# Kernel tuning notes

Measured on AMD Instinct MI355X. Metric: run time of the kernel, lower is better.

## Reference

```python
import jax, jax.numpy as jnp
import numpy as np
import math
from itertools import combinations

SEQ_LEN = 8
SET_SIZE = 3
IN_DIM = 2048
OUT_DIM = 1152
WAY = 5
SHOT = 5
N_QUERIES = 200
PE_SCALE = 0.1
LN_EPS = 1e-5
NEG_INF = -1e30

TUPLES = np.array(list(combinations(range(SEQ_LEN), SET_SIZE)), dtype=np.int32)  # [56, 3]
TUPLES_LEN = TUPLES.shape[0]


def _positional_encoding(d_model, max_len):
    position = np.arange(max_len)[:, None].astype(np.float32)
    div_term = np.exp(np.arange(0, d_model, 2).astype(np.float32) * -(math.log(10000.0) / d_model))
    pe = np.zeros((max_len, d_model), dtype=np.float32)
    pe[:, 0::2] = np.sin(position * div_term) * PE_SCALE
    pe[:, 1::2] = np.cos(position * div_term) * PE_SCALE
    return jnp.asarray(pe)

PE = _positional_encoding(IN_DIM, int(SEQ_LEN * 1.5))


def setup_inputs() -> dict:
    key = jax.random.key(0)
    ks = jax.random.split(key, 6)
    support_set = jax.random.normal(ks[0], (WAY * SHOT, SEQ_LEN, IN_DIM), dtype=jnp.float32)
    queries = jax.random.normal(ks[1], (N_QUERIES, SEQ_LEN, IN_DIM), dtype=jnp.float32)
    support_labels = jnp.repeat(jnp.arange(WAY, dtype=jnp.int32), SHOT)  # [25]
    Wk = jax.random.normal(ks[2], (IN_DIM * SET_SIZE, OUT_DIM), dtype=jnp.float32) * 0.02
    bk = jnp.zeros((OUT_DIM,), dtype=jnp.float32)
    Wv = jax.random.normal(ks[3], (IN_DIM * SET_SIZE, OUT_DIM), dtype=jnp.float32) * 0.02
    bv = jnp.zeros((OUT_DIM,), dtype=jnp.float32)
    ln_g = jnp.ones((OUT_DIM,), dtype=jnp.float32)
    ln_b = jnp.zeros((OUT_DIM,), dtype=jnp.float32)
    return {"support_set": support_set, "support_labels": support_labels, "queries": queries,
            "Wk": Wk, "bk": bk, "Wv": Wv, "bv": bv, "ln_g": ln_g, "ln_b": ln_b}


def _layernorm(x, g, b):
    mu = jnp.mean(x, axis=-1, keepdims=True)
    var = jnp.var(x, axis=-1, keepdims=True)
    return (x - mu) * jax.lax.rsqrt(var + LN_EPS) * g + b


def _tuple_features(x):
    # x: [N, SEQ_LEN, IN_DIM]; add PE (dropout is identity at inference), gather frame tuples.
    n = x.shape[0]
    x = x + PE[None, :x.shape[1], :]
    return x[:, TUPLES, :].reshape(n, TUPLES_LEN, SET_SIZE * IN_DIM)  # [N, 56, 6144]


def reference(support_set, support_labels, queries, Wk, bk, Wv, bv, ln_g, ln_b):
    n_q = queries.shape[0]
    s_feat = _tuple_features(support_set)   # [S, T, 6144]
    q_feat = _tuple_features(queries)       # [Q, T, 6144]

    sk = _layernorm(s_feat @ Wk + bk, ln_g, ln_b)  # [S, T, D]
    qk = _layernorm(q_feat @ Wk + bk, ln_g, ln_b)  # [Q, T, D]
    sv = s_feat @ Wv + bv                           # [S, T, D]
    qv = q_feat @ Wv + bv                           # [Q, T, D]

    # scores between every query tuple and every support tuple
    scores = jnp.einsum('qtd,skd->qtsk', qk, sk) / math.sqrt(OUT_DIM)  # [Q, T, S, T]

    # per-class masked softmax over (support clips of class c) x (support tuples)
    class_mask = support_labels[None, :] == jnp.arange(WAY, dtype=support_labels.dtype)[:, None]  # [WAY, S]
    masked = scores[None] + jnp.where(class_mask[:, None, None, :, None], 0.0, NEG_INF)  # [WAY, Q, T, S, T]
    attn = jax.nn.softmax(masked.reshape(WAY, n_q, TUPLES_LEN, -1), axis=-1)
    attn = attn.reshape(WAY, n_q, TUPLES_LEN, -1, TUPLES_LEN)  # [WAY, Q, T, S, T]

    proto = jnp.einsum('cqtsk,skd->cqtd', attn, sv)  # [WAY, Q, T, D]
    diff = qv[None] - proto                           # [WAY, Q, T, D]
    dist = -jnp.sum(diff * diff, axis=(2, 3)) / TUPLES_LEN  # [WAY, Q]
    return dist.T  # logits [Q, WAY]
```

## Files before the change

### kernel.cpp

```cpp
#include <hip/hip_runtime.h>
#include <math.h>

#define SEQ_LEN 8
#define IN_DIM 2048
#define OUT_DIM 1152
#define NTUP 56
#define NSUP 25
#define NQ 200
#define WAY 5
#define SFRAMES 200
#define NFRAMES 1800
#define SROWS 1400
#define QROWS 11200
#define AT_STRIDE 1440
#define KC 288
#define ALD 296

typedef __attribute__((ext_vector_type(8))) short short8;
typedef __attribute__((ext_vector_type(4))) float f32x4;

__device__ __constant__ int TUP[NTUP][3] = {
{0,1,2},{0,1,3},{0,1,4},{0,1,5},{0,1,6},{0,1,7},
{0,2,3},{0,2,4},{0,2,5},{0,2,6},{0,2,7},
{0,3,4},{0,3,5},{0,3,6},{0,3,7},
{0,4,5},{0,4,6},{0,4,7},
{0,5,6},{0,5,7},
{0,6,7},
{1,2,3},{1,2,4},{1,2,5},{1,2,6},{1,2,7},
{1,3,4},{1,3,5},{1,3,6},{1,3,7},
{1,4,5},{1,4,6},{1,4,7},
{1,5,6},{1,5,7},
{1,6,7},
{2,3,4},{2,3,5},{2,3,6},{2,3,7},
{2,4,5},{2,4,6},{2,4,7},
{2,5,6},{2,5,7},
{2,6,7},
{3,4,5},{3,4,6},{3,4,7},
{3,5,6},{3,5,7},
{3,6,7},
{4,5,6},{4,5,7},
{4,6,7},
{5,6,7}};

__device__ __forceinline__ unsigned short f2bf(float x) {
  union { float f; unsigned int u; } v; v.f = x;
  unsigned int r = v.u + 0x7fffu + ((v.u >> 16) & 1u);
  return (unsigned short)(r >> 16);
}
__device__ __forceinline__ float bf2f(unsigned short s) {
  union { float f; unsigned int u; } v; v.u = ((unsigned int)s) << 16;
  return v.f;
}

__device__ __forceinline__ void gll16(const void* g, void* l) {
  __builtin_amdgcn_global_load_lds(
      (const __attribute__((address_space(1))) unsigned int*)g,
      (__attribute__((address_space(3))) unsigned int*)l, 16, 0, 0);
}

#define VMCNT(N) asm volatile("s_waitcnt vmcnt(" #N ")" ::: "memory")

__device__ __forceinline__ void pbar() {
  asm volatile("" ::: "memory");
  __builtin_amdgcn_s_barrier();
  asm volatile("" ::: "memory");
}

#define APB_OFF   0UL
#define WT_OFF    7372800UL
#define PB_OFF    35684352UL
#define QKB_OFF   60567552UL
#define SKB_OFF   86372352UL
#define PVB_OFF   102039552UL
#define H_OFF     102061312UL
#define SVB_OFF   115402752UL
#define G2_OFF    118628352UL
#define SCB_OFF   119457792UL
#define G1B_OFF   151713792UL
#define QNORM_OFF 183969792UL
#define RANK_OFF  184014592UL

__global__ __launch_bounds__(256) void k_pre(const float* __restrict__ S,
                                             const float* __restrict__ Q,
                                             const float* __restrict__ Wk,
                                             const float* __restrict__ Wv,
                                             const int* __restrict__ labels,
                                             unsigned short* __restrict__ APb,
                                             unsigned short* __restrict__ WT,
                                             int* __restrict__ rank,
                                             float* __restrict__ outz) {
  __shared__ float t[32][33];
  int b = blockIdx.x, tid = threadIdx.x;
  if (b < NFRAMES) {
    int frame = b;
    int e8 = tid * 8;
    int pos = frame & 7;
    const float c0 = -logf(10000.0f) / (float)IN_DIM;
    float pe[8];
#pragma unroll
    for (int p = 0; p < 4; ++p) {
      float dt = expf((float)(e8 + 2 * p) * c0);
      float arg = (float)pos * dt;
      pe[2 * p] = sinf(arg) * 0.1f;
      pe[2 * p + 1] = cosf(arg) * 0.1f;
    }
    const float* src = (frame < SFRAMES) ? (S + (size_t)frame * IN_DIM + e8)
                                         : (Q + (size_t)(frame - SFRAMES) * IN_DIM + e8);
    float4 x0 = ((const float4*)src)[0], x1 = ((const float4*)src)[1];
    short8 o;
    o[0] = (short)f2bf(x0.x + pe[0]); o[1] = (short)f2bf(x0.y + pe[1]);
    o[2] = (short)f2bf(x0.z + pe[2]); o[3] = (short)f2bf(x0.w + pe[3]);
    o[4] = (short)f2bf(x1.x + pe[4]); o[5] = (short)f2bf(x1.y + pe[5]);
    o[6] = (short)f2bf(x1.z + pe[6]); o[7] = (short)f2bf(x1.w + pe[7]);
    *(short8*)(APb + (size_t)frame * IN_DIM + e8) = o;
  } else if (b < NFRAMES + 13824) {
    int z = b - NFRAMES;
    int bz = z / (64 * 36); int rem = z % (64 * 36);
    int by = rem / 64, bx = rem % 64;
    int w = bz / 3, j = bz % 3;
    const float* W = w ? Wv : Wk;
    int k0 = bx * 32, d0 = by * 32;
    int tx = tid & 31, ty = tid >> 5;
#pragma unroll
    for (int i = 0; i < 4; ++i) {
      int k = k0 + ty + i * 8;
      t[ty + i * 8][tx] = W[(size_t)(j * IN_DIM + k) * OUT_DIM + d0 + tx];
    }
    __syncthreads();
    int colbase = w * 3456 + j * 1152 + d0;
#pragma unroll
    for (int i = 0; i < 4; ++i) {
      int d = ty + i * 8;
      WT[(size_t)(colbase + d) * IN_DIM + k0 + tx] = f2bf(t[tx][d]);
    }
  } else {
    for (int i = tid; i < NQ * WAY; i += 256) outz[i] = 0.f;
    if (tid == 0) {
      for (int s = 0; s < NSUP; ++s) {
        int r = 0;
        for (int s2 = 0; s2 < NSUP; ++s2)
          r += (labels[s2] < labels[s]) || (labels[s2] == labels[s] && s2 < s);
        rank[s] = r;
      }
    }
  }
}

__device__ __forceinline__ void mfma_core256p(const short* a0p, const short* a1p,
                                              const short* a2p, const short* a3p,
                                              const short* b0p, const short* b1p,
                                              int K, short* lds, f32x4 (&acc)[8][4]) {
  int tid = threadIdx.x;
  int lane = tid & 63, wave = tid >> 6;
  int wm = wave >> 1, wn = wave & 1;
  int col = lane & 15, quad = lane >> 4;
  int kq8 = (quad ^ ((col >> 1) & 3)) * 8;
  const int nt = K >> 5;

#define STAGE(t, cb)                                 \
  do {                                               \
    short* buf_ = lds + (cb);                        \
    int k0_ = (t) << 5;                              \
    gll16(a0p + k0_, buf_ + (size_t)tid * 8);        \
    gll16(a1p + k0_, buf_ + (size_t)(tid + 256) * 8);\
    gll16(a2p + k0_, buf_ + (size_t)(tid + 512) * 8);\
    gll16(a3p + k0_, buf_ + (size_t)(tid + 768) * 8);\
    gll16(b0p + k0_, buf_ + 8192 + (size_t)tid * 8); \
    gll16(b1p + k0_, buf_ + 8192 + (size_t)(tid + 256) * 8);\
  } while (0)

  STAGE(0, 0);
  STAGE(1, 12288);
  VMCNT(6);
  pbar();
  int c0 = 0, c1 = 12288, c2 = 24576;
  for (int t = 0; t < nt; ++t) {
    if (t + 2 < nt) STAGE(t + 2, c2);
    const short* As = lds + c0;
    const short* Bs = As + 8192;
    short8 af[8], bf[4];
#pragma unroll
    for (int i = 0; i < 8; ++i)
      af[i] = *(const short8*)(As + (wm * 128 + i * 16 + col) * 32 + kq8);
#pragma unroll
    for (int j = 0; j < 4; ++j)
      bf[j] = *(const short8*)(Bs + (wn * 64 + j * 16 + col) * 32 + kq8);
    __builtin_amdgcn_s_setprio(1);
#pragma unroll
    for (int i = 0; i < 8; ++i)
#pragma unroll
      for (int j = 0; j < 4; ++j)
        acc[i][j] = __builtin_amdgcn_mfma_f32_16x16x32_bf16(af[i], bf[j], acc[i][j], 0, 0, 0);
    __builtin_amdgcn_s_setprio(0);
    if (t + 2 < nt)      VMCNT(6);
    else if (t + 1 < nt) VMCNT(0);
    pbar();
    int tmp = c0; c0 = c1; c1 = c2; c2 = tmp;
  }
#undef STAGE
}

__device__ __forceinline__ void mfma_core256(const short* __restrict__ A, int lda, int maxA,
                                             const short* __restrict__ B, int ldb, int maxB,
                                             int K, short* lds, f32x4 (&acc)[8][4]) {
  int tid = threadIdx.x;
  int rt_ = tid >> 2;
  int qo = ((tid & 3) ^ ((tid >> 3) & 3)) * 8;
  mfma_core256p(A + (size_t)min(rt_,       maxA) * lda + qo,
                A + (size_t)min(rt_ + 64,  maxA) * lda + qo,
                A + (size_t)min(rt_ + 128, maxA) * lda + qo,
                A + (size_t)min(rt_ + 192, maxA) * lda + qo,
                B + (size_t)min(rt_,       maxB) * ldb + qo,
                B + (size_t)min(rt_ + 64,  maxB) * ldb + qo,
                K, lds, acc);
}

__global__ __launch_bounds__(256, 2) void k_gemm1(const unsigned short* __restrict__ APb,
                                                  const unsigned short* __restrict__ WT,
                                                  unsigned short* __restrict__ Pb) {
  __shared__ short lds[36864];
  int o = blockIdx.x;
  int L = (o & 7) * 54 + (o >> 3);
  int rt = L / 54, ct = L % 54;
  int row0 = rt << 8, col0 = ct << 7;
  f32x4 acc[8][4];
#pragma unroll
  for (int i = 0; i < 8; ++i)
#pragma unroll
    for (int j = 0; j < 4; ++j) acc[i][j] = (f32x4)(0.f);
  mfma_core256((const short*)APb + (size_t)row0 * IN_DIM, IN_DIM, min(255, NFRAMES - 1 - row0),
               (const short*)WT + (size_t)col0 * IN_DIM, IN_DIM, 127,
               IN_DIM, lds, acc);
  int lane = threadIdx.x & 63, wave = threadIdx.x >> 6;
  int wm = wave >> 1, wn = wave & 1, col = lane & 15, quad = lane >> 4;
#pragma unroll
  for (int i = 0; i < 8; ++i)
#pragma unroll
    for (int r = 0; r < 4; ++r) {
      int gr = row0 + wm * 128 + i * 16 + quad * 4 + r;
      if (gr >= NFRAMES) continue;
#pragma unroll
      for (int j = 0; j < 4; ++j)
        Pb[(size_t)gr * 6912 + col0 + wn * 64 + j * 16 + col] = f2bf(acc[i][j][r]);
    }
}

__global__ __launch_bounds__(256) void k_pvb(const unsigned short* __restrict__ Pb,
                                             const float* __restrict__ bv,
                                             float* __restrict__ pvb) {
  int fr = blockIdx.x, tid = threadIdx.x;
  int wave = tid >> 6, lane = tid & 63;
  if (wave < 3) {
    const unsigned short* src = Pb + (size_t)fr * 6912 + 3456 + wave * 1152;
    float s = 0.f;
    for (int k = lane; k < OUT_DIM; k += 64) s += bf2f(src[k]) * bv[k];
#pragma unroll
    for (int o = 32; o; o >>= 1) s += __shfl_xor(s, o);
    if (lane == 0) pvb[fr * 3 + wave] = s;
  }
}

__global__ __launch_bounds__(256) void k_combine(const unsigned short* __restrict__ Pb,
                                                 const float* __restrict__ bk,
                                                 const float* __restrict__ bv,
                                                 const float* __restrict__ g,
                                                 const float* __restrict__ bb,
                                                 const int* __restrict__ rank,
                                                 unsigned short* __restrict__ SKb,
                                                 unsigned short* __restrict__ QKb,
                                                 unsigned short* __restrict__ SVb,
                                                 float* __restrict__ qnorm) {
  __shared__ short L[8 * 3456];
  int n = blockIdx.x, w = blockIdx.y;
  int tid = threadIdx.x;
  bool sup = n < NSUP;
  int fbase = sup ? n * SEQ_LEN : SFRAMES + (n - NSUP) * SEQ_LEN;
  for (int i = 0; i < 14; ++i) {
    int idx = tid + 256 * i;
    if (idx < 3456) {
      int fr = idx / 432, off = (idx - fr * 432) * 8;
      *(short8*)(L + fr * 3456 + off) =
          *(const short8*)(Pb + (size_t)(fbase + fr) * 6912 + w * 3456 + off);
    }
  }
  __syncthreads();
  int wave = tid >> 6, lane = tid & 63;
  const float* bias = w ? bv : bk;
  float2 bi[9], gg[9], bbv[9];
#pragma unroll
  for (int i = 0; i < 9; ++i) {
    int p = lane + 64 * i;
    bi[i] = *(const float2*)(bias + 2 * p);
    if (w == 0) {
      gg[i] = *(const float2*)(g + 2 * p);
      bbv[i] = *(const float2*)(bb + 2 * p);
    }
  }
  int obase = sup ? rank[n] * NTUP : (n - NSUP) * NTUP;
  const unsigned int* Lu = (const unsigned int*)L;
  for (int t = wave; t < NTUP; t += 4) {
    int b0 = (TUP[t][0] * 3456) >> 1;
    int b1 = (TUP[t][1] * 3456 + 1152) >> 1;
    int b2 = (TUP[t][2] * 3456 + 2304) >> 1;
    float va[18];
    float sum = 0.f, sq = 0.f;
#pragma unroll
    for (int i = 0; i < 9; ++i) {
      int p = lane + 64 * i;
      unsigned int u0 = Lu[b0 + p], u1 = Lu[b1 + p], u2 = Lu[b2 + p];
      float a = bf2f((unsigned short)u0) + bf2f((unsigned short)u1) +
                bf2f((unsigned short)u2) + bi[i].x;
      float b = bf2f((unsigned short)(u0 >> 16)) + bf2f((unsigned short)(u1 >> 16)) +
                bf2f((unsigned short)(u2 >> 16)) + bi[i].y;
      va[2 * i] = a; va[2 * i + 1] = b;
      sum += a + b;
      sq += a * a + b * b;
    }
#pragma unroll
    for (int o = 32; o; o >>= 1) {
      sum += __shfl_xor(sum, o);
      sq += __shfl_xor(sq, o);
    }
    int orow = obase + t;
    if (w == 0) {
      float mean = sum * (1.f / OUT_DIM);
      float var = sq * (1.f / OUT_DIM) - mean * mean;
      float inv = rsqrtf(var + 1e-5f);
      unsigned short* outp = (sup ? SKb : QKb) + (size_t)orow * OUT_DIM;
#pragma unroll
      for (int i = 0; i < 9; ++i) {
        int p = lane + 64 * i;
        unsigned int lo = f2bf((va[2 * i] - mean) * inv * gg[i].x + bbv[i].x);
        unsigned int hi = f2bf((va[2 * i + 1] - mean) * inv * gg[i].y + bbv[i].y);
        *(unsigned int*)(outp + 2 * p) = lo | (hi << 16);
      }
    } else if (sup) {
      unsigned short* outp = SVb + (size_t)orow * OUT_DIM;
#pragma unroll
      for (int i = 0; i < 9; ++i) {
        int p = lane + 64 * i;
        unsigned int lo = f2bf(va[2 * i]);
        unsigned int hi = f2bf(va[2 * i + 1]);
        *(unsigned int*)(outp + 2 * p) = lo | (hi << 16);
      }
    } else {
      if (lane == 0) qnorm[orow] = sq;
    }
  }
}

__global__ __launch_bounds__(256, 2) void k_rowgemm(const unsigned short* __restrict__ QKb,
                                                    const unsigned short* __restrict__ SKb,
                                                    const unsigned short* __restrict__ SVb,
                                                    const unsigned short* __restrict__ Pb,
                                                    unsigned short* __restrict__ SCb,
                                                    float* __restrict__ H,
                                                    unsigned short* __restrict__ G2) {
  __shared__ short lds[36864];
  int o = blockIdx.x;
  int xcd = o & 7, idx = o >> 3;
  int L = (xcd == 0 ? idx : 77 + (xcd - 1) * 76 + idx);
  f32x4 acc[8][4];
#pragma unroll
  for (int i = 0; i < 8; ++i)
#pragma unroll
    for (int j = 0; j < 4; ++j) acc[i][j] = (f32x4)(0.f);
  int lane = threadIdx.x & 63, wave = threadIdx.x >> 6;
  int wm = wave >> 1, wn = wave & 1, col = lane & 15, quad = lane >> 4;

  if (L < 484) {
    int rt = L / 11, ct = L % 11;
    int row0 = rt << 8, col0 = ct << 7;
    mfma_core256((const short*)QKb + (size_t)row0 * OUT_DIM, OUT_DIM, min(255, QROWS - 1 - row0),
                 (const short*)SKb + (size_t)col0 * OUT_DIM, OUT_DIM, min(127, SROWS - 1 - col0),
                 OUT_DIM, lds, acc);
    const float scl = 0.029462782549439483f;
#pragma unroll
    for (int i = 0; i < 8; ++i)
#pragma unroll
      for (int r = 0; r < 4; ++r) {
        int gr = row0 + wm * 128 + i * 16 + quad * 4 + r;
        if (gr >= QROWS) continue;
#pragma unroll
        for (int j = 0; j < 4; ++j) {
          int gc = col0 + wn * 64 + j * 16 + col;
          if (gc < SROWS) {
            int c = gc / 280;
            SCb[(size_t)gr * AT_STRIDE + gc + c * 8] = f2bf(acc[i][j][r] * scl);
          }
        }
      }
  } else if (L < 579) {
    int l = L - 484;
    int rt = l / 5, ct = l % 5;
    int row0 = rt << 8, col0 = ct << 7;
    int rt_ = threadIdx.x >> 2;
    int qo = ((threadIdx.x & 3) ^ ((threadIdx.x >> 3) & 3)) * 8;
    const short* Pv = (const short*)Pb + 3456;
    auto qaddr = [&](int v) {
      v = min(v, 4799);
      return Pv + (size_t)(SFRAMES + v / 3) * 6912 + (v % 3) * 1152 + qo;
    };
    auto saddr = [&](int v) {
      v = min(v, 599);
      return Pv + (size_t)(v / 3) * 6912 + (v % 3) * 1152 + qo;
    };
    mfma_core256p(qaddr(row0 + rt_), qaddr(row0 + rt_ + 64), qaddr(row0 + rt_ + 128),
                  qaddr(row0 + rt_ + 192), saddr(col0 + rt_), saddr(col0 + rt_ + 64),
                  OUT_DIM, lds, acc);
#pragma unroll
    for (int i = 0; i < 8; ++i)
#pragma unroll
      for (int r = 0; r < 4; ++r) {
        int gr = row0 + wm * 128 + i * 16 + quad * 4 + r;
        if (gr >= 4800) continue;
#pragma unroll
        for (int j = 0; j < 4; ++j) {
          int gc = col0 + wn * 64 + j * 16 + col;
          if (gc < 600) H[(size_t)gr * 640 + gc] = acc[i][j][r];
        }
      }
  } else {
    int l = L - 579;
    int c = l / 6, rem = l % 6;
    int rt = rem / 3, ct = rem % 3;
    int i0 = rt << 8, j0 = ct << 7;
    const short* base = (const short*)SVb + (size_t)c * 280 * OUT_DIM;
    mfma_core256(base + (size_t)i0 * OUT_DIM, OUT_DIM, 279 - i0,
                 base + (size_t)j0 * OUT_DIM, OUT_DIM, min(127, 279 - j0),
                 OUT_DIM, lds, acc);
    unsigned short* g2c = G2 + (size_t)c * KC * KC;
#pragma unroll
    for (int i = 0; i < 8; ++i)
#pragma unroll
      for (int r = 0; r < 4; ++r) {
        int gi = i0 + wm * 128 + i * 16 + quad * 4 + r;
        if (gi >= KC) continue;
#pragma unroll
        for (int j = 0; j < 4; ++j) {
          int gj = j0 + wn * 64 + j * 16 + col;
          if (gj < KC) g2c[(size_t)gi * KC + gj] = f2bf(acc[i][j][r]);
        }
      }
  }
}

__global__ __launch_bounds__(256) void k_g1asm(const float* __restrict__ H,
                                               const float* __restrict__ pvb,
                                               const float* __restrict__ bv,
                                               const int* __restrict__ rank,
                                               unsigned short* __restrict__ G1b) {
  __shared__ float Hs[24][24];
  __shared__ float M1[56][24];
  __shared__ float ubv[56], wbv[56];
  __shared__ float bb2s;
  __shared__ int inv[25];
  int qc = blockIdx.x, r = blockIdx.y;
  int tid = threadIdx.x;
  if (tid < 25) inv[rank[tid]] = tid;
  if (tid >= 64 && tid < 128) {
    int l = tid - 64;
    float s = 0.f;
    for (int k = l; k < OUT_DIM; k += 64) { float b = bv[k]; s += b * b; }
#pragma unroll
    for (int o = 32; o; o >>= 1) s += __shfl_xor(s, o);
    if (l == 0) bb2s = s;
  }
  __syncthreads();
  int n = inv[r];
  for (int i = tid; i < 576; i += 256) {
    int a = i / 24, b = i % 24;
    Hs[a][b] = H[(size_t)(qc * 24 + a) * 640 + n * 24 + b];
  }
  if (tid < 56) {
    float s = 0.f, w = 0.f;
#pragma unroll
    for (int j = 0; j < 3; ++j) {
      s += pvb[(SFRAMES + qc * 8 + TUP[tid][j]) * 3 + j];
      w += pvb[(n * 8 + TUP[tid][j]) * 3 + j];
    }
    ubv[tid] = s; wbv[tid] = w;
  }
  __syncthreads();
  for (int i = tid; i < 1344; i += 256) {
    int t = i / 24, b = i % 24;
    M1[t][b] = Hs[TUP[t][0] * 3 + 0][b] + Hs[TUP[t][1] * 3 + 1][b] + Hs[TUP[t][2] * 3 + 2][b];
  }
  __syncthreads();
  float bb2 = bb2s;
  int c = r / 5;
  size_t colbase = (size_t)c * KC + (r % 5) * 56;
  for (int i = tid; i < 3136; i += 256) {
    int t = i / 56, tp = i % 56;
    float v = M1[t][TUP[tp][0] * 3 + 0] + M1[t][TUP[tp][1] * 3 + 1] +
              M1[t][TUP[tp][2] * 3 + 2] + ubv[t] + wbv[tp] + bb2;
    G1b[(size_t)(qc * 56 + t) * AT_STRIDE + colbase + tp] = f2bf(v);
  }
}

__global__ __launch_bounds__(256) void k_attn(const unsigned short* __restrict__ SCb,
                                              const unsigned short* __restrict__ G1b,
                                              const unsigned short* __restrict__ G2,
                                              const float* __restrict__ qnorm,
                                              float* __restrict__ out) {
  __shared__ short attn[64 * ALD];
  __shared__ float T2n[64];
  __shared__ float Sarr[64];
  __shared__ float rowsum[64];
  __shared__ float val[64];
  int r0 = blockIdx.x * 64, c = blockIdx.y;
  int tid = threadIdx.x;

  int lr = tid >> 2, h = tid & 3;
  const unsigned short* ps = SCb + (size_t)(r0 + lr) * AT_STRIDE + c * KC;
  const unsigned short* pg = G1b + (size_t)(r0 + lr) * AT_STRIDE + c * KC;
  short8 sv[9];
  float mx = -INFINITY;
#pragma unroll
  for (int i = 0; i < 9; ++i) {
    int v = h * 9 + i;
    if (v < 35) {
      sv[i] = *(const short8*)(ps + v * 8);
#pragma unroll
      for (int j = 0; j < 8; ++j) mx = fmaxf(mx, bf2f((unsigned short)sv[i][j]));
    }
  }
  mx = fmaxf(mx, __shfl_xor(mx, 1));
  mx = fmaxf(mx, __shfl_xor(mx, 2));
  float sum = 0.f, t2 = 0.f;
#pragma unroll
  for (int i = 0; i < 9; ++i) {
    int v = h * 9 + i;
    if (v < 35) {
      short8 gv8 = *(const short8*)(pg + v * 8);
      short8 e8;
#pragma unroll
      for (int j = 0; j < 8; ++j) {
        float e = __expf(bf2f((unsigned short)sv[i][j]) - mx);
        sum += e;
        t2 += e * bf2f((unsigned short)gv8[j]);
        e8[j] = (short)f2bf(e);
      }
      *(short8*)(attn + lr * ALD + v * 8) = e8;
    } else {
      *(short8*)(attn + lr * ALD + v * 8) = (short8)0;
    }
  }
  sum += __shfl_xor(sum, 1); sum += __shfl_xor(sum, 2);
  t2 += __shfl_xor(t2, 1); t2 += __shfl_xor(t2, 2);
  if (h == 0) { Sarr[lr] = sum; T2n[lr] = t2; }
  if (tid < 64) rowsum[tid] = 0.f;
  __syncthreads();

  int lane = tid & 63, wave = tid >> 6;
  int col = lane & 15, quad = lane >> 4;
  const short* G2c = (const short*)G2 + (size_t)c * KC * KC;
  float part[4][4] = {};
  for (int j0 = 0; j0 < KC; j0 += 64) {
    int ncols = min(64, KC - j0);
    if (wave * 16 < ncols) {
      const short* brow = G2c + (size_t)(j0 + wave * 16 + col) * KC + quad * 8;
      f32x4 acc[4];
#pragma unroll
      for (int i = 0; i < 4; ++i) acc[i] = (f32x4)(0.f);
      for (int kq = 0; kq < 9; ++kq) {
        short8 bf = *(const short8*)(brow + kq * 32);
#pragma unroll
        for (int i = 0; i < 4; ++i) {
          short8 af = *(const short8*)(attn + (i * 16 + col) * ALD + kq * 32 + quad * 8);
          acc[i] = __builtin_amdgcn_mfma_f32_16x16x32_bf16(af, bf, acc[i], 0, 0, 0);
        }
      }
      int gcol = j0 + wave * 16 + col;
#pragma unroll
      for (int i = 0; i < 4; ++i)
#pragma unroll
        for (int r = 0; r < 4; ++r)
          part[i][r] += bf2f((unsigned short)attn[(i * 16 + quad * 4 + r) * ALD + gcol]) *
                        acc[i][r];
    }
  }
#pragma unroll
  for (int i = 0; i < 4; ++i)
#pragma unroll
    for (int r = 0; r < 4; ++r) {
      float s = part[i][r];
      s += __shfl_xor(s, 1); s += __shfl_xor(s, 2);
      s += __shfl_xor(s, 4); s += __shfl_xor(s, 8);
      if (col == 0) atomicAdd(&rowsum[i * 16 + quad * 4 + r], s);
    }
  __syncthreads();

  if (tid < 64) {
    float S = Sarr[tid], invS = 1.f / S;
    val[tid] = qnorm[r0 + tid] - 2.f * T2n[tid] * invS + rowsum[tid] * invS * invS;
  }
  __syncthreads();
  if (tid < 3) {
    int q = r0 / NTUP + tid;
    int lo = max(q * NTUP, r0), hi = min(q * NTUP + NTUP, r0 + 64);
    if (lo < hi && q < NQ) {
      float s = 0.f;
      for (int r = lo; r < hi; ++r) s += val[r - r0];
      atomicAdd(&out[q * WAY + c], -s * (1.f / NTUP));
    }
  }
}

extern "C" void kernel_launch(void* const* d_in, const int* in_sizes, int n_in,
                              void* d_out, int out_size, void* d_ws, size_t ws_size,
                              hipStream_t stream) {
  const float* support = (const float*)d_in[0];
  const int* labels = (const int*)d_in[1];
  const float* queries = (const float*)d_in[2];
  const float* Wk = (const float*)d_in[3];
  const float* bk = (const float*)d_in[4];
  const float* Wv = (const float*)d_in[5];
  const float* bv = (const float*)d_in[6];
  const float* ln_g = (const float*)d_in[7];
  const float* ln_b = (const float*)d_in[8];
  float* out = (float*)d_out;
  char* w8 = (char*)d_ws;

  unsigned short* APb = (unsigned short*)(w8 + APB_OFF);
  unsigned short* WT = (unsigned short*)(w8 + WT_OFF);
  unsigned short* Pb = (unsigned short*)(w8 + PB_OFF);
  unsigned short* QKb = (unsigned short*)(w8 + QKB_OFF);
  unsigned short* SKb = (unsigned short*)(w8 + SKB_OFF);
  float* PVB = (float*)(w8 + PVB_OFF);
  float* H = (float*)(w8 + H_OFF);
  unsigned short* SVb = (unsigned short*)(w8 + SVB_OFF);
  unsigned short* G2 = (unsigned short*)(w8 + G2_OFF);
  unsigned short* SCb = (unsigned short*)(w8 + SCB_OFF);
  unsigned short* G1b = (unsigned short*)(w8 + G1B_OFF);
  float* QNORM = (float*)(w8 + QNORM_OFF);
  int* RANK = (int*)(w8 + RANK_OFF);

  k_pre<<<dim3(NFRAMES + 13824 + 1), dim3(256), 0, stream>>>(support, queries, Wk, Wv,
                                                             labels, APb, WT, RANK, out);
  k_gemm1<<<dim3(432), dim3(256), 0, stream>>>(APb, WT, Pb);
  k_pvb<<<dim3(NFRAMES), dim3(256), 0, stream>>>(Pb, bv, PVB);
  k_combine<<<dim3(225, 2), dim3(256), 0, stream>>>(Pb, bk, bv, ln_g, ln_b, RANK,
                                                    SKb, QKb, SVb, QNORM);
  k_rowgemm<<<dim3(609), dim3(256), 0, stream>>>(QKb, SKb, SVb, Pb, SCb, H, G2);
  k_g1asm<<<dim3(200, 25), dim3(256), 0, stream>>>(H, PVB, bv, RANK, G1b);
  k_attn<<<dim3(175, 5), dim3(256), 0, stream>>>(SCb, G1b, G2, QNORM, out);
}
```

Baseline: 364.6 us.

## Fuse G1 assembly into attention kernel and fold pvb into combine

Removes the k_g1asm kernel, which wrote a large bf16 G1 matrix (11200x1440) to global memory, and k_attn no longer reads it back. k_attn now loads the relevant H slices into shared memory, builds per-row M1 partial sums, and computes each G1 entry on the fly from M1, ubv and wbv inside the softmax loop. The per-frame pvb dot products move from a separate kernel into k_combine, reusing the Pb rows it already stages in LDS. This cuts two launches and a large global write and read, at the cost of more shared memory and extra arithmetic and LDS gathers in k_attn, which may lower occupancy.

```diff
diff --git a/kernel.cpp b/kernel.cpp
--- a/kernel.cpp
+++ b/kernel.cpp
@@ -76,7 +76,6 @@
 #define SVB_OFF   115402752UL
 #define G2_OFF    118628352UL
 #define SCB_OFF   119457792UL
-#define G1B_OFF   151713792UL
 #define QNORM_OFF 183969792UL
 #define RANK_OFF  184014592UL
 
@@ -245,21 +244,6 @@
     }
 }
 
-__global__ __launch_bounds__(256) void k_pvb(const unsigned short* __restrict__ Pb,
-                                             const float* __restrict__ bv,
-                                             float* __restrict__ pvb) {
-  int fr = blockIdx.x, tid = threadIdx.x;
-  int wave = tid >> 6, lane = tid & 63;
-  if (wave < 3) {
-    const unsigned short* src = Pb + (size_t)fr * 6912 + 3456 + wave * 1152;
-    float s = 0.f;
-    for (int k = lane; k < OUT_DIM; k += 64) s += bf2f(src[k]) * bv[k];
-#pragma unroll
-    for (int o = 32; o; o >>= 1) s += __shfl_xor(s, o);
-    if (lane == 0) pvb[fr * 3 + wave] = s;
-  }
-}
-
 __global__ __launch_bounds__(256) void k_combine(const unsigned short* __restrict__ Pb,
                                                  const float* __restrict__ bk,
                                                  const float* __restrict__ bv,
@@ -269,7 +253,8 @@
                                                  unsigned short* __restrict__ SKb,
                                                  unsigned short* __restrict__ QKb,
                                                  unsigned short* __restrict__ SVb,
-                                                 float* __restrict__ qnorm) {
+                                                 float* __restrict__ qnorm,
+                                                 float* __restrict__ pvb) {
   __shared__ short L[8 * 3456];
   int n = blockIdx.x, w = blockIdx.y;
   int tid = threadIdx.x;
@@ -285,6 +270,17 @@
   }
   __syncthreads();
   int wave = tid >> 6, lane = tid & 63;
+  if (w == 1) {
+    for (int d = wave; d < 24; d += 4) {
+      int f = d / 3, j = d - (d / 3) * 3;
+      const unsigned short* p = (const unsigned short*)L + f * 3456 + j * 1152;
+      float s = 0.f;
+      for (int k = lane; k < OUT_DIM; k += 64) s += bf2f(p[k]) * bv[k];
+#pragma unroll
+      for (int o = 32; o; o >>= 1) s += __shfl_xor(s, o);
+      if (lane == 0) pvb[(fbase + f) * 3 + j] = s;
+    }
+  }
   const float* bias = w ? bv : bk;
   float2 bi[9], gg[9], bbv[9];
 #pragma unroll
@@ -445,75 +441,81 @@
   }
 }
 
-__global__ __launch_bounds__(256) void k_g1asm(const float* __restrict__ H,
-                                               const float* __restrict__ pvb,
-                                               const float* __restrict__ bv,
-                                               const int* __restrict__ rank,
-                                               unsigned short* __restrict__ G1b) {
-  __shared__ float Hs[24][24];
-  __shared__ float M1[56][24];
-  __shared__ float ubv[56], wbv[56];
-  __shared__ float bb2s;
-  __shared__ int inv[25];
-  int qc = blockIdx.x, r = blockIdx.y;
-  int tid = threadIdx.x;
-  if (tid < 25) inv[rank[tid]] = tid;
-  if (tid >= 64 && tid < 128) {
-    int l = tid - 64;
-    float s = 0.f;
-    for (int k = l; k < OUT_DIM; k += 64) { float b = bv[k]; s += b * b; }
-#pragma unroll
-    for (int o = 32; o; o >>= 1) s += __shfl_xor(s, o);
-    if (l == 0) bb2s = s;
-  }
-  __syncthreads();
-  int n = inv[r];
-  for (int i = tid; i < 576; i += 256) {
-    int a = i / 24, b = i % 24;
-    Hs[a][b] = H[(size_t)(qc * 24 + a) * 640 + n * 24 + b];
-  }
-  if (tid < 56) {
-    float s = 0.f, w = 0.f;
-#pragma unroll
-    for (int j = 0; j < 3; ++j) {
-      s += pvb[(SFRAMES + qc * 8 + TUP[tid][j]) * 3 + j];
-      w += pvb[(n * 8 + TUP[tid][j]) * 3 + j];
-    }
-    ubv[tid] = s; wbv[tid] = w;
-  }
-  __syncthreads();
-  for (int i = tid; i < 1344; i += 256) {
-    int t = i / 24, b = i % 24;
-    M1[t][b] = Hs[TUP[t][0] * 3 + 0][b] + Hs[TUP[t][1] * 3 + 1][b] + Hs[TUP[t][2] * 3 + 2][b];
-  }
-  __syncthreads();
-  float bb2 = bb2s;
-  int c = r / 5;
-  size_t colbase = (size_t)c * KC + (r % 5) * 56;
-  for (int i = tid; i < 3136; i += 256) {
-    int t = i / 56, tp = i % 56;
-    float v = M1[t][TUP[tp][0] * 3 + 0] + M1[t][TUP[tp][1] * 3 + 1] +
-              M1[t][TUP[tp][2] * 3 + 2] + ubv[t] + wbv[tp] + bb2;
-    G1b[(size_t)(qc * 56 + t) * AT_STRIDE + colbase + tp] = f2bf(v);
-  }
-}
-
 __global__ __launch_bounds__(256) void k_attn(const unsigned short* __restrict__ SCb,
-                                              const unsigned short* __restrict__ G1b,
+                                              const float* __restrict__ H,
+                                              const float* __restrict__ pvb,
+                                              const float* __restrict__ bv,
+                                              const int* __restrict__ rank,
                                               const unsigned short* __restrict__ G2,
                                               const float* __restrict__ qnorm,
                                               float* __restrict__ out) {
   __shared__ short attn[64 * ALD];
+  __shared__ float M1[64][120];
+  __shared__ float wbvs[5][56];
+  __shared__ float ubv[64];
   __shared__ float T2n[64];
   __shared__ float Sarr[64];
   __shared__ float rowsum[64];
   __shared__ float val[64];
+  __shared__ int inv[25];
+  __shared__ float bb2s;
   int r0 = blockIdx.x * 64, c = blockIdx.y;
   int tid = threadIdx.x;
+  float* Hs = (float*)attn;
+
+  if (tid < 25) inv[rank[tid]] = tid;
+  __syncthreads();
+
+  int qcA = r0 / 56;
+  int qcB = min(qcA + 1, NQ - 1);
+  for (int i = tid; i < 5760; i += 256) {
+    int a = i / 120, bcol = i - (i / 120) * 120;
+    int s5 = bcol / 24, b = bcol - s5 * 24;
+    int qc = (a < 24) ? qcA : qcB;
+    int ar = (a < 24) ? a : a - 24;
+    int n = inv[c * 5 + s5];
+    Hs[a * 120 + bcol] = H[(size_t)(qc * 24 + ar) * 640 + n * 24 + b];
+  }
+  if (tid < 64) {
+    int gr = r0 + tid;
+    int qc = gr / 56, t = gr - qc * 56;
+    float s = 0.f;
+#pragma unroll
+    for (int j = 0; j < 3; ++j)
+      s += pvb[(SFRAMES + qc * 8 + TUP[t][j]) * 3 + j];
+    ubv[tid] = s;
+  }
+  if (tid >= 192) {
+    int l = tid - 192;
+    float s = 0.f;
+    for (int k = l; k < OUT_DIM; k += 64) { float b = bv[k]; s += b * b; }
+#pragma unroll
+    for (int o = 32; o; o >>= 1) s += __shfl_xor(s, o);
+    if (l == 0) bb2s = s;
+  }
+  __syncthreads();
+  for (int i = tid; i < 280; i += 256) {
+    int s5 = i / 56, tp = i - s5 * 56;
+    int n = inv[c * 5 + s5];
+    float s = bb2s;
+#pragma unroll
+    for (int j = 0; j < 3; ++j)
+      s += pvb[(n * 8 + TUP[tp][j]) * 3 + j];
+    wbvs[s5][tp] = s;
+  }
+  for (int i = tid; i < 7680; i += 256) {
+    int lr = i / 120, bcol = i - (i / 120) * 120;
+    int gr = r0 + lr;
+    int qc = gr / 56, t = gr - qc * 56;
+    int ro = (qc == qcA) ? 0 : 24;
+    M1[lr][bcol] = Hs[(ro + TUP[t][0] * 3 + 0) * 120 + bcol] +
+                   Hs[(ro + TUP[t][1] * 3 + 1) * 120 + bcol] +
+                   Hs[(ro + TUP[t][2] * 3 + 2) * 120 + bcol];
+  }
+  __syncthreads();
 
   int lr = tid >> 2, h = tid & 3;
   const unsigned short* ps = SCb + (size_t)(r0 + lr) * AT_STRIDE + c * KC;
-  const unsigned short* pg = G1b + (size_t)(r0 + lr) * AT_STRIDE + c * KC;
   short8 sv[9];
   float mx = -INFINITY;
 #pragma unroll
@@ -528,17 +530,22 @@
   mx = fmaxf(mx, __shfl_xor(mx, 1));
   mx = fmaxf(mx, __shfl_xor(mx, 2));
   float sum = 0.f, t2 = 0.f;
+  float gb = ubv[lr];
 #pragma unroll
   for (int i = 0; i < 9; ++i) {
     int v = h * 9 + i;
     if (v < 35) {
-      short8 gv8 = *(const short8*)(pg + v * 8);
+      int s5 = v / 7, tpb = (v - s5 * 7) * 8;
+      const float* m = &M1[lr][s5 * 24];
       short8 e8;
 #pragma unroll
       for (int j = 0; j < 8; ++j) {
+        int tp = tpb + j;
         float e = __expf(bf2f((unsigned short)sv[i][j]) - mx);
+        float g1 = m[TUP[tp][0] * 3 + 0] + m[TUP[tp][1] * 3 + 1] +
+                   m[TUP[tp][2] * 3 + 2] + gb + wbvs[s5][tp];
         sum += e;
-        t2 += e * bf2f((unsigned short)gv8[j]);
+        t2 += e * g1;
         e8[j] = (short)f2bf(e);
       }
       *(short8*)(attn + lr * ALD + v * 8) = e8;
@@ -632,17 +639,14 @@
   unsigned short* SVb = (unsigned short*)(w8 + SVB_OFF);
   unsigned short* G2 = (unsigned short*)(w8 + G2_OFF);
   unsigned short* SCb = (unsigned short*)(w8 + SCB_OFF);
-  unsigned short* G1b = (unsigned short*)(w8 + G1B_OFF);
   float* QNORM = (float*)(w8 + QNORM_OFF);
   int* RANK = (int*)(w8 + RANK_OFF);
 
   k_pre<<<dim3(NFRAMES + 13824 + 1), dim3(256), 0, stream>>>(support, queries, Wk, Wv,
                                                              labels, APb, WT, RANK, out);
   k_gemm1<<<dim3(432), dim3(256), 0, stream>>>(APb, WT, Pb);
-  k_pvb<<<dim3(NFRAMES), dim3(256), 0, stream>>>(Pb, bv, PVB);
   k_combine<<<dim3(225, 2), dim3(256), 0, stream>>>(Pb, bk, bv, ln_g, ln_b, RANK,
-                                                    SKb, QKb, SVb, QNORM);
+                                                    SKb, QKb, SVb, QNORM, PVB);
   k_rowgemm<<<dim3(609), dim3(256), 0, stream>>>(QKb, SKb, SVb, Pb, SCb, H, G2);
-  k_g1asm<<<dim3(200, 25), dim3(256), 0, stream>>>(H, PVB, bv, RANK, G1b);
-  k_attn<<<dim3(175, 5), dim3(256), 0, stream>>>(SCb, G1b, G2, QNORM, out);
-}
+  k_attn<<<dim3(175, 5), dim3(256), 0, stream>>>(SCb, H, PVB, bv, RANK, G2, QNORM, out);
+}
```

Result: slower. 375.1 us (+2.9%).
